# Performance work log

Hardware: AMD Instinct MI355X
Metric: run time of the kernel (lower is better)

Reference implementation:

```python
import jax, jax.numpy as jnp
import numpy as np

S_MUL, V_MUL = 32, 16          # 32x0e + 16x1o
NODE_DIM = S_MUL + 3 * V_MUL   # 80
LATENT = 128
INV_SQRT3 = 1.0 / np.sqrt(3.0)          # wigner 3j (1,1,0) / (0,1,1) / (1,0,1) factor
C_SCALAR = np.float32(1.0 / np.sqrt(48.0))   # path_norm 'element': fan into 0e = 32*1 + 16*1
C_VECTOR = np.float32(np.sqrt(3.0 / 48.0))   # irrep dim 3 / fan 48 for 1o output


def setup_inputs() -> dict:
    rng = np.random.default_rng(0)
    B, n_atoms, radius = 2048, 32, 5.0
    N = B * n_atoms
    # atoms uniform in a 10A cube -> ~300 edges per 32-atom graph at r=5
    pos_g = rng.uniform(0.0, 10.0, size=(B, n_atoms, 3)).astype(np.float32)
    diff = pos_g[:, :, None, :] - pos_g[:, None, :, :]
    d2 = (diff * diff).sum(-1)
    mask = (d2 <= radius * radius) & (d2 > 0.0)   # same predicate as build_radius_graph
    b_idx, i_idx, j_idx = np.nonzero(mask)
    edge_index = np.stack([b_idx * n_atoms + i_idx, b_idx * n_atoms + j_idx]).astype(np.int32)
    pos = pos_g.reshape(N, 3)
    z = rng.integers(0, 100, size=N).astype(np.int32)
    batch = np.repeat(np.arange(B, dtype=np.int32), n_atoms)
    L = 3  # num_layers

    def w(*shape, scale=1.0):
        return jnp.asarray((rng.standard_normal(shape) * scale).astype(np.float32))

    return dict(
        pos=jnp.asarray(pos), z=jnp.asarray(z), batch=jnp.asarray(batch),
        edge_index=jnp.asarray(edge_index), num_graphs=B,
        emb=w(100, S_MUL),                      # nn.Embedding(100, 32) ~ N(0,1)
        W_s2n=w(S_MUL, S_MUL),                  # e3nn Linear 32x0e -> 32x0e path
        W1=w(L, S_MUL, S_MUL),                  # tp path 0e x 0e -> 0e
        W2=w(L, S_MUL, V_MUL),                  # tp path 0e x 1o -> 1o
        W3=w(L, V_MUL, V_MUL),                  # tp path 1o x 0e -> 1o
        W4=w(L, V_MUL, S_MUL),                  # tp path 1o x 1o -> 0e
        Ws=w(L, S_MUL, S_MUL),                  # e3nn Linear scalar block
        Wv=w(L, V_MUL, V_MUL),                  # e3nn Linear vector block
        Wr1=w(NODE_DIM, 256, scale=1.0 / np.sqrt(NODE_DIM)), br1=jnp.zeros((256,), jnp.float32),
        Wr2=w(256, LATENT, scale=1.0 / np.sqrt(256.0)), br2=jnp.zeros((LATENT,), jnp.float32),
    )


def _forward(pos, emb, W_s2n, W1, W2, W3, W4, Ws, Wv, Wr1, br1, Wr2, br2,
             z, batch, edge_index, num_graphs):
    N = pos.shape[0]
    src, dst = edge_index[0], edge_index[1]
    # atom embedding -> node irreps (only 0e->0e path exists; vectors start at 0)
    s = (emb[z] @ W_s2n) * np.float32(1.0 / np.sqrt(S_MUL))   # (N, 32)
    v = jnp.zeros((N, V_MUL, 3), pos.dtype)                   # (N, 16, 3)
    # spherical harmonics, normalize=True, 'component': Y0 = 1, Y1 = sqrt(3) * r_hat
    rij = pos[dst] - pos[src]                                 # (E, 3)
    sh1 = np.float32(np.sqrt(3.0)) * rij / jnp.linalg.norm(rij, axis=-1, keepdims=True)
    for l in range(W1.shape[0]):
        ss, vs = s[src], v[src]                               # gather (E,32), (E,16,3)
        # FullyConnectedTensorProduct(node, sh, node), uvw weights, sh0 == 1
        m_s = C_SCALAR * (jnp.einsum('eu,uw->ew', ss, W1[l])
                          + INV_SQRT3 * jnp.einsum('eui,ei,uw->ew', vs, sh1, W4[l]))
        m_v = (C_VECTOR * INV_SQRT3) * (jnp.einsum('eu,ei,uw->ewi', ss, sh1, W2[l])
                                        + jnp.einsum('eui,uw->ewi', vs, W3[l]))
        a_s = jax.ops.segment_sum(m_s, dst, num_segments=N)   # index_add_ scatter
        a_v = jax.ops.segment_sum(m_v, dst, num_segments=N)
        # e3nn Linear (per-irrep block, 1/sqrt(fan_in)) then relu on FULL feature (as in source)
        h_s = jax.nn.relu((a_s @ Ws[l]) * np.float32(1.0 / np.sqrt(S_MUL)))
        h_v = jax.nn.relu(jnp.einsum('nvi,vw->nwi', a_v, Wv[l]) * np.float32(1.0 / np.sqrt(V_MUL)))
        s, v = s + h_s, v + h_v                               # residual
    x = jnp.concatenate([s, v.reshape(N, V_MUL * 3)], axis=-1)  # (N, 80)
    hg = jax.ops.segment_sum(x, batch, num_segments=num_graphs) # sum-pool per graph
    return jax.nn.relu(hg @ Wr1 + br1) @ Wr2 + br2              # (B, latent)


def reference(pos, emb, W_s2n, W1, W2, W3, W4, Ws, Wv, Wr1, br1, Wr2, br2,
              z, batch, edge_index, num_graphs):
    return _forward(pos, emb, W_s2n, W1, W2, W3, W4, Ws, Wv, Wr1, br1, Wr2, br2,
                    z, batch, edge_index, num_graphs)
```

## Files before the change

kernel.cpp:

```cpp
#include <hip/hip_runtime.h>
#include <math.h>

typedef __attribute__((ext_vector_type(8))) short bf16x8;
typedef __attribute__((ext_vector_type(4))) float f32x4;

#define SQRT3F     1.7320508075688772f
#define SCALE_T    0.17677669529663687f
#define SCALE_M1   0.025515518153991442f
#define SCALE_M2   0.014731391274719739f
#define SCALE_M34  0.036084391824351615f

#define FSTR 40

__device__ __forceinline__ ushort f2bf(float f) {
    union { float f; unsigned u; } v; v.f = f;
    unsigned u = v.u;
    return (ushort)((u + 0x7FFFu + ((u >> 16) & 1u)) >> 16);
}
__device__ __forceinline__ float bf2f(ushort h) {
    union { unsigned u; float f; } v; v.u = ((unsigned)h) << 16;
    return v.f;
}
__device__ __forceinline__ unsigned packbf(float lo, float hi) {
    return (unsigned)f2bf(lo) | ((unsigned)f2bf(hi) << 16);
}
__device__ __forceinline__ unsigned cvtpk(float lo, float hi) {
    unsigned r;
    asm("v_cvt_pk_bf16_f32 %0, %1, %2" : "=v"(r) : "v"(lo), "v"(hi));
    return r;
}
__device__ __forceinline__ void pl32(unsigned &a, unsigned &b) {
    auto r = __builtin_amdgcn_permlane32_swap(a, b, false, false);
    a = r[0]; b = r[1];
}
__device__ __forceinline__ void pl16(unsigned &a, unsigned &b) {
    auto r = __builtin_amdgcn_permlane16_swap(a, b, false, false);
    a = r[0]; b = r[1];
}
__device__ __forceinline__ f32x4 mfma(bf16x8 a, bf16x8 b, f32x4 c) {
    return __builtin_amdgcn_mfma_f32_16x16x32_bf16(a, b, c, 0, 0, 0);
}
__device__ __forceinline__ void makeFrags(f32x4 T0, f32x4 T1, f32x4 T2,
                                          bf16x8 &f0, bf16x8 &f1) {
    unsigned p0 = packbf(T0[0], T0[1]), p1 = packbf(T0[2], T0[3]);
    unsigned q0 = packbf(T1[0], T1[1]), q1 = packbf(T1[2], T1[3]);
    unsigned s0 = packbf(T2[0], T2[1]), s1 = packbf(T2[2], T2[3]);
    pl32(p0, q0); pl16(p0, q0);
    pl32(p1, q1); pl16(p1, q1);
    unsigned z0 = 0u, z1 = 0u;
    pl32(s0, z0); pl16(s0, z0);
    pl32(s1, z1); pl16(s1, z1);
    union { bf16x8 v; unsigned u[4]; } r;
    r.u[0] = p0; r.u[1] = p1; r.u[2] = q0; r.u[3] = q1; f0 = r.v;
    r.u[0] = s0; r.u[1] = s1; r.u[2] = z0; r.u[3] = z1; f1 = r.v;
}
__device__ __forceinline__ void rmw4(ushort* F, int c, int n0, f32x4 h) {
    uint2* p = (uint2*)&F[c*FSTR + n0];
    uint2 o = *p;
    float f0 = bf2f((ushort)(o.x      )) + fmaxf(h[0], 0.f);
    float f1 = bf2f((ushort)(o.x >> 16)) + fmaxf(h[1], 0.f);
    float f2 = bf2f((ushort)(o.y      )) + fmaxf(h[2], 0.f);
    float f3 = bf2f((ushort)(o.y >> 16)) + fmaxf(h[3], 0.f);
    uint2 w;
    w.x = cvtpk(f0, f1);
    w.y = cvtpk(f2, f3);
    *p = w;
}

__global__ void prep_kernel(const float* __restrict__ emb,
                            const float* __restrict__ W_s2n,
                            const float* __restrict__ W1, const float* __restrict__ W2,
                            const float* __restrict__ W3, const float* __restrict__ W4,
                            const float* __restrict__ Ws, const float* __restrict__ Wv,
                            ushort* __restrict__ Tbf, ushort* __restrict__ Mbf)
{
    int idx = blockIdx.x * blockDim.x + threadIdx.x;
    if (idx < 3200) {
        int r = idx >> 5, c = idx & 31;
        float acc = 0.f;
        for (int k = 0; k < 32; ++k) acc += emb[r*32 + k] * W_s2n[k*32 + c];
        Tbf[idx] = f2bf(acc * SCALE_T);
        return;
    }
    idx -= 3200;
    if (idx < 3*48*64) {
        int lyr = idx / 3072, rem = idx % 3072;
        int row = rem >> 6, u = rem & 63;
        float val = 0.f;
        if (row < 32) {
            int w = row;
            if (u < 32) {
                float a = 0.f;
                for (int k = 0; k < 32; ++k)
                    a += W1[lyr*1024 + u*32 + k] * Ws[lyr*1024 + k*32 + w];
                val = a * SCALE_M1;
            } else if (u < 48) {
                int uu = u - 32; float a = 0.f;
                for (int k = 0; k < 32; ++k)
                    a += W4[lyr*512 + uu*32 + k] * Ws[lyr*1024 + k*32 + w];
                val = a * SCALE_M2;
            }
        } else {
            int w = row - 32;
            if (u < 32) {
                float a = 0.f;
                for (int k = 0; k < 16; ++k)
                    a += W2[lyr*512 + u*16 + k] * Wv[lyr*256 + k*16 + w];
                val = a * SCALE_M34;
            } else if (u < 48) {
                int uu = u - 32; float a = 0.f;
                for (int k = 0; k < 16; ++k)
                    a += W3[lyr*256 + uu*16 + k] * Wv[lyr*256 + k*16 + w];
                val = a * SCALE_M34;
            }
        }
        Mbf[lyr*3072 + row*64 + u] = f2bf(val);
    }
}

__global__ __launch_bounds__(256)
void gnn_kernel(const float* __restrict__ pos, const int* __restrict__ z,
                const ushort* __restrict__ Tbf, const ushort* __restrict__ Mbf,
                const float* __restrict__ Wr1, const float* __restrict__ br1,
                const float* __restrict__ Wr2, const float* __restrict__ br2,
                float* __restrict__ out, int B)
{
    __shared__ __align__(16) char smem[26880];
    ushort* featA = (ushort*)smem;
    float*  hgl   = (float*)(smem + 25600);
    float*  h1    = (float*)smem;
    float*  red   = (float*)(smem + 4096);

    const int tid = threadIdx.x;
    const int wv = tid >> 6, l = tid & 63;
    const int g  = blockIdx.x*4 + wv;
    ushort* F  = featA + wv*80*FSTR;

    for (int i = l; i < 48*(FSTR/2); i += 64) ((uint*)(F + 32*FSTR))[i] = 0;

    {
        int n = l & 31, h = l >> 5;
        int zg = z[g*32 + n];
        uint4 t0 = *(const uint4*)(Tbf + zg*32 + h*16);
        uint4 t1 = *(const uint4*)(Tbf + zg*32 + h*16 + 8);
        unsigned ua[8] = {t0.x, t0.y, t0.z, t0.w, t1.x, t1.y, t1.z, t1.w};
        #pragma unroll
        for (int q = 0; q < 8; ++q) {
            F[(h*16 + 2*q    )*FSTR + n] = (ushort)ua[q];
            F[(h*16 + 2*q + 1)*FSTR + n] = (ushort)(ua[q] >> 16);
        }
    }

    const int ln = l & 15, kq = l >> 4;
    bf16x8 adjf[4][2];
    {
        const int k0 = kq*8;
        #pragma unroll
        for (int nt = 0; nt < 2; ++nt) {
            int ng = g*32 + nt*16 + ln;
            float px = pos[3*ng], py = pos[3*ng+1], pz = pos[3*ng+2];
            union { bf16x8 v; ushort s[8]; } o[4];
            #pragma unroll
            for (int jj = 0; jj < 8; ++jj) {
                int j = g*32 + k0 + jj;
                float dx = __fsub_rn(px, pos[3*j]);
                float dy = __fsub_rn(py, pos[3*j+1]);
                float dz = __fsub_rn(pz, pos[3*j+2]);
                float d2 = __fadd_rn(__fadd_rn(__fmul_rn(dx,dx), __fmul_rn(dy,dy)),
                                     __fmul_rn(dz,dz));
                bool on = (d2 <= 25.0f) && (d2 > 0.0f);
                float rinv = on ? rsqrtf(d2) * SQRT3F : 0.f;
                o[0].s[jj] = on ? (ushort)0x3F80 : (ushort)0;
                o[1].s[jj] = f2bf(dx * rinv);
                o[2].s[jj] = f2bf(dy * rinv);
                o[3].s[jj] = f2bf(dz * rinv);
            }
            #pragma unroll
            for (int w = 0; w < 4; ++w) adjf[w][nt] = o[w].v;
        }
    }

    const f32x4 z4 = {0.f, 0.f, 0.f, 0.f};

    for (int lay = 0; lay < 3; ++lay) {
        const ushort* Mg = Mbf + lay*3072;
        bf16x8 fs0 = *(const bf16x8*)&F[(     ln)*FSTR + kq*8];
        bf16x8 fs1 = *(const bf16x8*)&F[(16 + ln)*FSTR + kq*8];
        bf16x8 fv0 = *(const bf16x8*)&F[(32 + ln)*FSTR + kq*8];
        bf16x8 fv1 = *(const bf16x8*)&F[(48 + ln)*FSTR + kq*8];
        bf16x8 fv2 = *(const bf16x8*)&F[(64 + ln)*FSTR + kq*8];
        bf16x8 bmS0[2], bmS1[2], bmV[2];
        #pragma unroll
        for (int kc = 0; kc < 2; ++kc) {
            bmS0[kc] = *(const bf16x8*)&Mg[(     ln)*64 + kc*32 + kq*8];
            bmS1[kc] = *(const bf16x8*)&Mg[(16 + ln)*64 + kc*32 + kq*8];
            bmV [kc] = *(const bf16x8*)&Mg[(32 + ln)*64 + kc*32 + kq*8];
        }

        bf16x8 agf[2][2];

        #pragma unroll
        for (int nt = 0; nt < 2; ++nt) {
            f32x4 T0 = mfma(fs0, adjf[0][nt], z4);
            f32x4 T1 = mfma(fs1, adjf[0][nt], z4);
            f32x4 T2 = mfma(fv2, adjf[3][nt], z4);
            T2 = mfma(fv1, adjf[2][nt], T2);
            T2 = mfma(fv0, adjf[1][nt], T2);
            makeFrags(T0, T1, T2, agf[nt][0], agf[nt][1]);
        }
        f32x4 hs[2][2] = {{z4, z4}, {z4, z4}};
        #pragma unroll
        for (int kc = 0; kc < 2; ++kc)
            #pragma unroll
            for (int mt = 0; mt < 2; ++mt) {
                hs[mt][0] = mfma(agf[mt][kc], bmS0[kc], hs[mt][0]);
                hs[mt][1] = mfma(agf[mt][kc], bmS1[kc], hs[mt][1]);
            }
        #pragma unroll
        for (int mt = 0; mt < 2; ++mt)
            #pragma unroll
            for (int wt = 0; wt < 2; ++wt)
                rmw4(F, wt*16 + ln, mt*16 + kq*4, hs[mt][wt]);

        #pragma unroll
        for (int i = 0; i < 3; ++i) {
            bf16x8 fvi = (i == 0) ? fv0 : (i == 1) ? fv1 : fv2;
            #pragma unroll
            for (int nt = 0; nt < 2; ++nt) {
                f32x4 T0 = mfma(fs0, adjf[1+i][nt], z4);
                f32x4 T1 = mfma(fs1, adjf[1+i][nt], z4);
                f32x4 T2 = mfma(fvi, adjf[0][nt], z4);
                makeFrags(T0, T1, T2, agf[nt][0], agf[nt][1]);
            }
            f32x4 hv[2] = {z4, z4};
            #pragma unroll
            for (int kc = 0; kc < 2; ++kc)
                #pragma unroll
                for (int mt = 0; mt < 2; ++mt)
                    hv[mt] = mfma(agf[mt][kc], bmV[kc], hv[mt]);
            #pragma unroll
            for (int mt = 0; mt < 2; ++mt)
                rmw4(F, 32 + i*16 + ln, mt*16 + kq*4, hv[mt]);
        }
    }

    for (int f = l; f < 80; f += 64) {
        const ushort* row;
        if (f < 32) row = &F[f*FSTR];
        else { int c = f - 32, w = c/3, i = c - 3*w; row = &F[(32 + i*16 + w)*FSTR]; }
        const uint* r32 = (const uint*)row;
        float acc = 0.f;
        #pragma unroll
        for (int q = 0; q < 16; ++q) {
            uint u = r32[q];
            acc += bf2f((ushort)u) + bf2f((ushort)(u >> 16));
        }
        hgl[wv*80 + f] = acc;
    }
    __syncthreads();

    {
        const int w = tid;
        float acc0 = br1[w];
        float acc1 = acc0, acc2 = acc0, acc3 = acc0;
        #pragma unroll 4
        for (int f = 0; f < 80; ++f) {
            float wvv = Wr1[f*256 + w];
            acc0 = fmaf(hgl[0*80 + f], wvv, acc0);
            acc1 = fmaf(hgl[1*80 + f], wvv, acc1);
            acc2 = fmaf(hgl[2*80 + f], wvv, acc2);
            acc3 = fmaf(hgl[3*80 + f], wvv, acc3);
        }
        h1[0*256 + w] = fmaxf(acc0, 0.f);
        h1[1*256 + w] = fmaxf(acc1, 0.f);
        h1[2*256 + w] = fmaxf(acc2, 0.f);
        h1[3*256 + w] = fmaxf(acc3, 0.f);
    }
    __syncthreads();
    {
        const int g0 = blockIdx.x * 4;
        const int w2 = tid & 127, kh = tid >> 7;
        const float4* h1v = (const float4*)h1;
        float s0 = 0.f, s1 = 0.f, s2 = 0.f, s3 = 0.f;
        #pragma unroll 2
        for (int k4 = kh*32; k4 < kh*32 + 32; ++k4) {
            float4 hA = h1v[0*64 + k4];
            float4 hB = h1v[1*64 + k4];
            float4 hC = h1v[2*64 + k4];
            float4 hD = h1v[3*64 + k4];
            int k = k4 * 4;
            float m0 = Wr2[(size_t)(k+0)*128 + w2];
            float m1 = Wr2[(size_t)(k+1)*128 + w2];
            float m2 = Wr2[(size_t)(k+2)*128 + w2];
            float m3 = Wr2[(size_t)(k+3)*128 + w2];
            s0 = fmaf(hA.x,m0, fmaf(hA.y,m1, fmaf(hA.z,m2, fmaf(hA.w,m3, s0))));
            s1 = fmaf(hB.x,m0, fmaf(hB.y,m1, fmaf(hB.z,m2, fmaf(hB.w,m3, s1))));
            s2 = fmaf(hC.x,m0, fmaf(hC.y,m1, fmaf(hC.z,m2, fmaf(hC.w,m3, s2))));
            s3 = fmaf(hD.x,m0, fmaf(hD.y,m1, fmaf(hD.z,m2, fmaf(hD.w,m3, s3))));
        }
        if (kh) {
            red[0*128 + w2] = s0; red[1*128 + w2] = s1;
            red[2*128 + w2] = s2; red[3*128 + w2] = s3;
        }
        __syncthreads();
        if (!kh) {
            float b = br2[w2];
            out[(size_t)(g0+0)*128 + w2] = s0 + red[0*128 + w2] + b;
            out[(size_t)(g0+1)*128 + w2] = s1 + red[1*128 + w2] + b;
            out[(size_t)(g0+2)*128 + w2] = s2 + red[2*128 + w2] + b;
            out[(size_t)(g0+3)*128 + w2] = s3 + red[3*128 + w2] + b;
        }
    }
}

extern "C" void kernel_launch(void* const* d_in, const int* in_sizes, int n_in,
                              void* d_out, int out_size, void* d_ws, size_t ws_size,
                              hipStream_t stream)
{
    const float* pos   = (const float*)d_in[0];
    const int*   z     = (const int*)d_in[1];
    const float* emb   = (const float*)d_in[5];
    const float* W_s2n = (const float*)d_in[6];
    const float* W1    = (const float*)d_in[7];
    const float* W2    = (const float*)d_in[8];
    const float* W3    = (const float*)d_in[9];
    const float* W4    = (const float*)d_in[10];
    const float* Ws    = (const float*)d_in[11];
    const float* Wv    = (const float*)d_in[12];
    const float* Wr1   = (const float*)d_in[13];
    const float* br1   = (const float*)d_in[14];
    const float* Wr2   = (const float*)d_in[15];
    const float* br2   = (const float*)d_in[16];
    float* out = (float*)d_out;

    const int B = out_size / 128;

    char* p = (char*)d_ws;
    ushort* Tbf = (ushort*)p;  p += 6400;
    ushort* Mbf = (ushort*)p;  p += 18432;

    const int prep_total = 3200 + 3*48*64;
    prep_kernel<<<(prep_total + 255) / 256, 256, 0, stream>>>(
        emb, W_s2n, W1, W2, W3, W4, Ws, Wv, Tbf, Mbf);

    gnn_kernel<<<B / 4, 256, 0, stream>>>(pos, z, Tbf, Mbf,
                                          Wr1, br1, Wr2, br2, out, B);
}
```

Baseline: 112.8 us.

## Keep node features in fp32 registers across layers instead of LDS bf16 round-trips

Node feature state (scalar and vector blocks) is now held per lane in fp32 accumulator registers that match the MFMA output layout. Each layer rebuilds the bf16 A-operand fragments through permlane swaps instead of reading them from LDS, and the residual-plus-ReLU update happens in registers rather than as an LDS read-modify-write. The features are written back to LDS once, after the last layer, for pooling. The bf16 packing also switches from software rounding to the hardware v_cvt_pk_bf16_f32 instruction, and the residual stays in fp32 between layers, which slightly changes numerics. The cost is higher register pressure and more permlane work per layer.

```diff
diff --git a/kernel.cpp b/kernel.cpp
--- a/kernel.cpp
+++ b/kernel.cpp
@@ -21,9 +21,6 @@
     union { unsigned u; float f; } v; v.u = ((unsigned)h) << 16;
     return v.f;
 }
-__device__ __forceinline__ unsigned packbf(float lo, float hi) {
-    return (unsigned)f2bf(lo) | ((unsigned)f2bf(hi) << 16);
-}
 __device__ __forceinline__ unsigned cvtpk(float lo, float hi) {
     unsigned r;
     asm("v_cvt_pk_bf16_f32 %0, %1, %2" : "=v"(r) : "v"(lo), "v"(hi));
@@ -40,31 +37,27 @@
 __device__ __forceinline__ f32x4 mfma(bf16x8 a, bf16x8 b, f32x4 c) {
     return __builtin_amdgcn_mfma_f32_16x16x32_bf16(a, b, c, 0, 0, 0);
 }
-__device__ __forceinline__ void makeFrags(f32x4 T0, f32x4 T1, f32x4 T2,
-                                          bf16x8 &f0, bf16x8 &f1) {
-    unsigned p0 = packbf(T0[0], T0[1]), p1 = packbf(T0[2], T0[3]);
-    unsigned q0 = packbf(T1[0], T1[1]), q1 = packbf(T1[2], T1[3]);
-    unsigned s0 = packbf(T2[0], T2[1]), s1 = packbf(T2[2], T2[3]);
+__device__ __forceinline__ bf16x8 makeFrag(f32x4 T0, f32x4 T1) {
+    unsigned p0 = cvtpk(T0[0], T0[1]), p1 = cvtpk(T0[2], T0[3]);
+    unsigned q0 = cvtpk(T1[0], T1[1]), q1 = cvtpk(T1[2], T1[3]);
     pl32(p0, q0); pl16(p0, q0);
     pl32(p1, q1); pl16(p1, q1);
+    union { bf16x8 v; unsigned u[4]; } r;
+    r.u[0] = p0; r.u[1] = p1; r.u[2] = q0; r.u[3] = q1;
+    return r.v;
+}
+__device__ __forceinline__ bf16x8 makeFragZ(f32x4 T2) {
+    unsigned s0 = cvtpk(T2[0], T2[1]), s1 = cvtpk(T2[2], T2[3]);
     unsigned z0 = 0u, z1 = 0u;
     pl32(s0, z0); pl16(s0, z0);
     pl32(s1, z1); pl16(s1, z1);
     union { bf16x8 v; unsigned u[4]; } r;
-    r.u[0] = p0; r.u[1] = p1; r.u[2] = q0; r.u[3] = q1; f0 = r.v;
-    r.u[0] = s0; r.u[1] = s1; r.u[2] = z0; r.u[3] = z1; f1 = r.v;
-}
-__device__ __forceinline__ void rmw4(ushort* F, int c, int n0, f32x4 h) {
-    uint2* p = (uint2*)&F[c*FSTR + n0];
-    uint2 o = *p;
-    float f0 = bf2f((ushort)(o.x      )) + fmaxf(h[0], 0.f);
-    float f1 = bf2f((ushort)(o.x >> 16)) + fmaxf(h[1], 0.f);
-    float f2 = bf2f((ushort)(o.y      )) + fmaxf(h[2], 0.f);
-    float f3 = bf2f((ushort)(o.y >> 16)) + fmaxf(h[3], 0.f);
-    uint2 w;
-    w.x = cvtpk(f0, f1);
-    w.y = cvtpk(f2, f3);
-    *p = w;
+    r.u[0] = s0; r.u[1] = s1; r.u[2] = z0; r.u[3] = z1;
+    return r.v;
+}
+__device__ __forceinline__ void accRelu(f32x4 &S, f32x4 h) {
+    S[0] += fmaxf(h[0], 0.f); S[1] += fmaxf(h[1], 0.f);
+    S[2] += fmaxf(h[2], 0.f); S[3] += fmaxf(h[3], 0.f);
 }
 
 __global__ void prep_kernel(const float* __restrict__ emb,
@@ -135,8 +128,7 @@
     const int wv = tid >> 6, l = tid & 63;
     const int g  = blockIdx.x*4 + wv;
     ushort* F  = featA + wv*80*FSTR;
-
-    for (int i = l; i < 48*(FSTR/2); i += 64) ((uint*)(F + 32*FSTR))[i] = 0;
+    const int ln = l & 15, kq = l >> 4;
 
     {
         int n = l & 31, h = l >> 5;
@@ -151,7 +143,23 @@
         }
     }
 
-    const int ln = l & 15, kq = l >> 4;
+    f32x4 Ss[2][2];
+    f32x4 Sv[2][3];
+    #pragma unroll
+    for (int mt = 0; mt < 2; ++mt) {
+        #pragma unroll
+        for (int wt = 0; wt < 2; ++wt) {
+            uint2 d = *(const uint2*)&F[(wt*16 + ln)*FSTR + mt*16 + kq*4];
+            Ss[mt][wt][0] = bf2f((ushort)(d.x      ));
+            Ss[mt][wt][1] = bf2f((ushort)(d.x >> 16));
+            Ss[mt][wt][2] = bf2f((ushort)(d.y      ));
+            Ss[mt][wt][3] = bf2f((ushort)(d.y >> 16));
+        }
+        #pragma unroll
+        for (int i = 0; i < 3; ++i)
+            Sv[mt][i] = (f32x4){0.f, 0.f, 0.f, 0.f};
+    }
+
     bf16x8 adjf[4][2];
     {
         const int k0 = kq*8;
@@ -184,11 +192,11 @@
 
     for (int lay = 0; lay < 3; ++lay) {
         const ushort* Mg = Mbf + lay*3072;
-        bf16x8 fs0 = *(const bf16x8*)&F[(     ln)*FSTR + kq*8];
-        bf16x8 fs1 = *(const bf16x8*)&F[(16 + ln)*FSTR + kq*8];
-        bf16x8 fv0 = *(const bf16x8*)&F[(32 + ln)*FSTR + kq*8];
-        bf16x8 fv1 = *(const bf16x8*)&F[(48 + ln)*FSTR + kq*8];
-        bf16x8 fv2 = *(const bf16x8*)&F[(64 + ln)*FSTR + kq*8];
+        bf16x8 fs0 = makeFrag(Ss[0][0], Ss[1][0]);
+        bf16x8 fs1 = makeFrag(Ss[0][1], Ss[1][1]);
+        bf16x8 fv0 = makeFrag(Sv[0][0], Sv[1][0]);
+        bf16x8 fv1 = makeFrag(Sv[0][1], Sv[1][1]);
+        bf16x8 fv2 = makeFrag(Sv[0][2], Sv[1][2]);
         bf16x8 bmS0[2], bmS1[2], bmV[2];
         #pragma unroll
         for (int kc = 0; kc < 2; ++kc) {
@@ -206,7 +214,8 @@
             f32x4 T2 = mfma(fv2, adjf[3][nt], z4);
             T2 = mfma(fv1, adjf[2][nt], T2);
             T2 = mfma(fv0, adjf[1][nt], T2);
-            makeFrags(T0, T1, T2, agf[nt][0], agf[nt][1]);
+            agf[nt][0] = makeFrag(T0, T1);
+            agf[nt][1] = makeFragZ(T2);
         }
         f32x4 hs[2][2] = {{z4, z4}, {z4, z4}};
         #pragma unroll
@@ -220,7 +229,7 @@
         for (int mt = 0; mt < 2; ++mt)
             #pragma unroll
             for (int wt = 0; wt < 2; ++wt)
-                rmw4(F, wt*16 + ln, mt*16 + kq*4, hs[mt][wt]);
+                accRelu(Ss[mt][wt], hs[mt][wt]);
 
         #pragma unroll
         for (int i = 0; i < 3; ++i) {
@@ -230,7 +239,8 @@
                 f32x4 T0 = mfma(fs0, adjf[1+i][nt], z4);
                 f32x4 T1 = mfma(fs1, adjf[1+i][nt], z4);
                 f32x4 T2 = mfma(fvi, adjf[0][nt], z4);
-                makeFrags(T0, T1, T2, agf[nt][0], agf[nt][1]);
+                agf[nt][0] = makeFrag(T0, T1);
+                agf[nt][1] = makeFragZ(T2);
             }
             f32x4 hv[2] = {z4, z4};
             #pragma unroll
@@ -240,7 +250,25 @@
                     hv[mt] = mfma(agf[mt][kc], bmV[kc], hv[mt]);
             #pragma unroll
             for (int mt = 0; mt < 2; ++mt)
-                rmw4(F, 32 + i*16 + ln, mt*16 + kq*4, hv[mt]);
+                accRelu(Sv[mt][i], hv[mt]);
+        }
+    }
+
+    #pragma unroll
+    for (int mt = 0; mt < 2; ++mt) {
+        #pragma unroll
+        for (int wt = 0; wt < 2; ++wt) {
+            uint2 w;
+            w.x = cvtpk(Ss[mt][wt][0], Ss[mt][wt][1]);
+            w.y = cvtpk(Ss[mt][wt][2], Ss[mt][wt][3]);
+            *(uint2*)&F[(wt*16 + ln)*FSTR + mt*16 + kq*4] = w;
+        }
+        #pragma unroll
+        for (int i = 0; i < 3; ++i) {
+            uint2 w;
+            w.x = cvtpk(Sv[mt][i][0], Sv[mt][i][1]);
+            w.y = cvtpk(Sv[mt][i][2], Sv[mt][i][3]);
+            *(uint2*)&F[(32 + i*16 + ln)*FSTR + mt*16 + kq*4] = w;
         }
     }
 
```

Result: faster. 110.3 us (-2.2%).
